# Kernel optimization log

Measured on AMD Instinct MI355X. Metric: run time of the kernel, lower is better.

The kernel has to match this reference:

```python
import jax, jax.numpy as jnp
import numpy as np

# Graph sizes: users -> items ('ui') and users -> tags ('ut'), plus reverse etypes.
N_U, N_I, N_T, D = 100000, 50000, 20000, 128
E_UI, E_UT = 500000, 300000


def setup_inputs() -> dict:
    key = jax.random.key(0)
    k = jax.random.split(key, 7)
    return {
        "h_u": jax.random.normal(k[0], (N_U, D), jnp.float32),
        "h_i": jax.random.normal(k[1], (N_I, D), jnp.float32),
        "h_t": jax.random.normal(k[2], (N_T, D), jnp.float32),
        "ui_src": jax.random.randint(k[3], (E_UI,), 0, N_U, jnp.int32),
        "ui_dst": jax.random.randint(k[4], (E_UI,), 0, N_I, jnp.int32),
        "ut_src": jax.random.randint(k[5], (E_UT,), 0, N_U, jnp.int32),
        "ut_dst": jax.random.randint(k[6], (E_UT,), 0, N_T, jnp.int32),
    }


def _seg_sum(x, idx, n):
    return jax.ops.segment_sum(x, idx, num_segments=n)


def _deg(idx, n):
    # in-degree, clamped to min 1 (as torch .clamp(min=1))
    return jnp.clip(_seg_sum(jnp.ones(idx.shape, jnp.float32), idx, n), 1.0, None)


def reference(h_u, h_i, h_t, ui_src, ui_dst, ut_src, ut_dst):
    NORM_2 = -1.0  # default norm_2 arg
    # forward pass: copy_u('h') + sum per etype, then 1/in_degree normalization on dst
    rst_i = _seg_sum(h_u[ui_src], ui_dst, N_I) / _deg(ui_dst, N_I)[:, None]  # [N_I, D]
    rst_t = _seg_sum(h_u[ut_src], ut_dst, N_T) / _deg(ut_dst, N_T)[:, None]  # [N_T, D]
    # backward pass: multi_update_all over reverse etypes, 'sum' cross-etype reducer
    bsrc = _seg_sum(rst_i[ui_dst], ui_src, N_U) + _seg_sum(rst_t[ut_dst], ut_src, N_U)
    # in_degrees_b: per-etype clamped degrees summed across reverse etypes
    deg_b = _deg(ui_src, N_U) + _deg(ut_src, N_U)
    bsrc = bsrc * (deg_b ** NORM_2)[:, None]
    # rst is the LAST etype's normalized dst result ('ut' -> tags)
    return bsrc, rst_t
```

## Files before the change

### kernel.cpp

```cpp
#include <hip/hip_runtime.h>

#define NU 100000
#define NI 50000
#define NT 20000
#define DD 128
#define EUI 500000
#define EUT 300000

#define B_I   0
#define B_T   (NI)
#define B_UUI (NI + NT)
#define B_UUT (NI + NT + NU)
#define NSCAN (NI + NT + NU + NU)
#define TOTAL_E (2 * (EUI + EUT))

#define BPB   512
#define NB    ((NSCAN + BPB - 1) / BPB)
#define CH    2048
#define NBLK  ((TOTAL_E + CH - 1) / CH)
#define NT3   176
#define NCVT  ((NU * DD / 8 + 255) / 256)

__device__ __forceinline__ unsigned bfpack(float a, float b) {
    unsigned ua = __float_as_uint(a), ub = __float_as_uint(b);
    ua = (ua + 0x7FFFu + ((ua >> 16) & 1u)) >> 16;
    ub = (ub + 0x7FFFu + ((ub >> 16) & 1u)) >> 16;
    return ua | (ub << 16);
}
__device__ __forceinline__ void bacc(unsigned p, float& a, float& b) {
    a += __uint_as_float(p << 16);
    b += __uint_as_float(p & 0xFFFF0000u);
}

typedef float f4_t __attribute__((ext_vector_type(4)));
__device__ __forceinline__ void nts4(float4* p, float x, float y, float z, float w) {
    f4_t v; v.x = x; v.y = y; v.z = z; v.w = w;
    __builtin_nontemporal_store(v, reinterpret_cast<f4_t*>(p));
}

__device__ __forceinline__ int bucket_of(int e,
        const int* __restrict__ ui_src, const int* __restrict__ ui_dst,
        const int* __restrict__ ut_src, const int* __restrict__ ut_dst) {
    if (e < EUI)               return B_I   + ui_dst[e];
    if (e < 2 * EUI)           return B_UUI + ui_src[e - EUI];
    if (e < 2 * EUI + EUT)     return B_T   + ut_dst[e - 2 * EUI];
    return B_UUT + ut_src[e - 2 * EUI - EUT];
}

__device__ __forceinline__ void entry_of(int e,
        const int* __restrict__ ui_src, const int* __restrict__ ui_dst,
        const int* __restrict__ ut_src, const int* __restrict__ ut_dst,
        int& bucket, int& val) {
    if (e < EUI)               { bucket = B_I   + ui_dst[e];               val = ui_src[e]; }
    else if (e < 2 * EUI)      { int j = e - EUI;           bucket = B_UUI + ui_src[j]; val = ui_dst[j]; }
    else if (e < 2 * EUI + EUT){ int j = e - 2 * EUI;       bucket = B_T   + ut_dst[j]; val = ut_src[j]; }
    else                       { int j = e - 2 * EUI - EUT; bucket = B_UUT + ut_src[j]; val = ut_dst[j]; }
}

__global__ void k_cvthist(const float4* __restrict__ in, uint4* __restrict__ out,
                          const int* __restrict__ ui_src, const int* __restrict__ ui_dst,
                          const int* __restrict__ ut_src, const int* __restrict__ ut_dst,
                          int* __restrict__ gbin) {
    __shared__ int h[NB];
    if (blockIdx.x < NCVT) {
        int t = blockIdx.x * 256 + threadIdx.x;
        if (t < NU * DD / 8) {
            float4 a = in[t * 2 + 0];
            float4 b = in[t * 2 + 1];
            uint4 o;
            o.x = bfpack(a.x, a.y); o.y = bfpack(a.z, a.w);
            o.z = bfpack(b.x, b.y); o.w = bfpack(b.z, b.w);
            out[t] = o;
        }
        return;
    }
    int b = blockIdx.x - NCVT, t = threadIdx.x;
    for (int i = t; i < NB; i += 256) h[i] = 0;
    __syncthreads();
    int e0 = b * CH;
    int e1 = min(e0 + CH, TOTAL_E);
    for (int e = e0 + t; e < e1; e += 256)
        atomicAdd(&h[bucket_of(e, ui_src, ui_dst, ut_src, ut_dst) >> 9], 1);
    __syncthreads();
    for (int i = t; i < NB; i += 256)
        if (h[i]) atomicAdd(&gbin[i], h[i]);
}

__global__ void k_scan528(const int* __restrict__ gbin,
                          int* __restrict__ gstart, int* __restrict__ cursor) {
    __shared__ int tsum[256];
    int t = threadIdx.x;
    int i = t * 3;
    int v0 = 0, v1 = 0, v2 = 0;
    if (t < NT3) { v0 = gbin[i]; v1 = gbin[i + 1]; v2 = gbin[i + 2]; }
    int s = v0 + v1 + v2;
    tsum[t] = s;
    __syncthreads();
    for (int o = 1; o < 256; o <<= 1) {
        int x = (t >= o) ? tsum[t - o] : 0;
        __syncthreads();
        tsum[t] += x;
        __syncthreads();
    }
    int base = tsum[t] - s;
    if (t < NT3) {
        gstart[i] = base;                cursor[i] = base;
        gstart[i + 1] = base + v0;       cursor[i + 1] = base + v0;
        gstart[i + 2] = base + v0 + v1;  cursor[i + 2] = base + v0 + v1;
    }
    if (t == 255) gstart[NB] = tsum[255];
}

__global__ void k_scatterbin2(const int* __restrict__ ui_src, const int* __restrict__ ui_dst,
                              const int* __restrict__ ut_src, const int* __restrict__ ut_dst,
                              int* __restrict__ cursor, unsigned* __restrict__ binned) {
    __shared__ int h[NB];
    int b = blockIdx.x, t = threadIdx.x;
    for (int i = t; i < NB; i += 256) h[i] = 0;
    __syncthreads();
    int e0 = b * CH;
    int e1 = min(e0 + CH, TOTAL_E);
    for (int e = e0 + t; e < e1; e += 256)
        atomicAdd(&h[bucket_of(e, ui_src, ui_dst, ut_src, ut_dst) >> 9], 1);
    __syncthreads();
    for (int i = t; i < NB; i += 256) {
        int c = h[i];
        if (c) h[i] = atomicAdd(&cursor[i], c);
    }
    __syncthreads();
    for (int e = e0 + t; e < e1; e += 256) {
        int bucket, val;
        entry_of(e, ui_src, ui_dst, ut_src, ut_dst, bucket, val);
        int pos = atomicAdd(&h[bucket >> 9], 1);
        binned[pos] = ((unsigned)(bucket & (BPB - 1)) << 17) | (unsigned)val;
    }
}

__global__ void k_fine(const unsigned* __restrict__ binned, const int* __restrict__ gstart,
                       int* __restrict__ off, int* __restrict__ edges) {
    __shared__ int cnt[BPB];
    __shared__ int tsum[256];
    int b = blockIdx.x, t = threadIdx.x;
    cnt[t] = 0; cnt[t + 256] = 0;
    __syncthreads();
    int s = gstart[b], e = gstart[b + 1];
    for (int i = s + t; i < e; i += 256) atomicAdd(&cnt[binned[i] >> 17], 1);
    __syncthreads();
    int v0 = cnt[2 * t], v1 = cnt[2 * t + 1];
    int ps = v0 + v1;
    tsum[t] = ps;
    __syncthreads();
    for (int o = 1; o < 256; o <<= 1) {
        int x = (t >= o) ? tsum[t - o] : 0;
        __syncthreads();
        tsum[t] += x;
        __syncthreads();
    }
    int base = s + tsum[t] - ps;
    int g0 = b * BPB + 2 * t;
    if (g0 < NSCAN) off[g0] = base;
    if (g0 + 1 < NSCAN) off[g0 + 1] = base + v0;
    __syncthreads();
    cnt[2 * t] = base;
    cnt[2 * t + 1] = base + v0;
    __syncthreads();
    for (int i = s + t; i < e; i += 256) {
        unsigned v = binned[i];
        int pos = atomicAdd(&cnt[v >> 17], 1);
        edges[pos] = (int)(v & 0x1FFFFu);
    }
}

__device__ __forceinline__ void gacc16(const uint4* __restrict__ feat,
                                       const int* __restrict__ edges,
                                       int start, int end, int c,
                                       float& a0, float& a1, float& a2, float& a3,
                                       float& a4, float& a5, float& a6, float& a7) {
    for (int base = start; base < end; base += 16) {
        int n = end - base; if (n > 16) n = 16;
        int eidx = (c < n) ? edges[base + c] : 0;
        int k = 0;
        for (; k + 8 <= n; k += 8) {
            int s0 = __shfl(eidx, k + 0, 16), s1 = __shfl(eidx, k + 1, 16);
            int s2 = __shfl(eidx, k + 2, 16), s3 = __shfl(eidx, k + 3, 16);
            int s4 = __shfl(eidx, k + 4, 16), s5 = __shfl(eidx, k + 5, 16);
            int s6 = __shfl(eidx, k + 6, 16), s7 = __shfl(eidx, k + 7, 16);
            uint4 p0 = feat[(size_t)s0 * 16 + c], p1 = feat[(size_t)s1 * 16 + c];
            uint4 p2 = feat[(size_t)s2 * 16 + c], p3 = feat[(size_t)s3 * 16 + c];
            uint4 p4 = feat[(size_t)s4 * 16 + c], p5 = feat[(size_t)s5 * 16 + c];
            uint4 p6 = feat[(size_t)s6 * 16 + c], p7 = feat[(size_t)s7 * 16 + c];
            bacc(p0.x, a0, a1); bacc(p0.y, a2, a3); bacc(p0.z, a4, a5); bacc(p0.w, a6, a7);
            bacc(p1.x, a0, a1); bacc(p1.y, a2, a3); bacc(p1.z, a4, a5); bacc(p1.w, a6, a7);
            bacc(p2.x, a0, a1); bacc(p2.y, a2, a3); bacc(p2.z, a4, a5); bacc(p2.w, a6, a7);
            bacc(p3.x, a0, a1); bacc(p3.y, a2, a3); bacc(p3.z, a4, a5); bacc(p3.w, a6, a7);
            bacc(p4.x, a0, a1); bacc(p4.y, a2, a3); bacc(p4.z, a4, a5); bacc(p4.w, a6, a7);
            bacc(p5.x, a0, a1); bacc(p5.y, a2, a3); bacc(p5.z, a4, a5); bacc(p5.w, a6, a7);
            bacc(p6.x, a0, a1); bacc(p6.y, a2, a3); bacc(p6.z, a4, a5); bacc(p6.w, a6, a7);
            bacc(p7.x, a0, a1); bacc(p7.y, a2, a3); bacc(p7.z, a4, a5); bacc(p7.w, a6, a7);
        }
        for (; k + 2 <= n; k += 2) {
            int s0 = __shfl(eidx, k + 0, 16), s1 = __shfl(eidx, k + 1, 16);
            uint4 p0 = feat[(size_t)s0 * 16 + c], p1 = feat[(size_t)s1 * 16 + c];
            bacc(p0.x, a0, a1); bacc(p0.y, a2, a3); bacc(p0.z, a4, a5); bacc(p0.w, a6, a7);
            bacc(p1.x, a0, a1); bacc(p1.y, a2, a3); bacc(p1.z, a4, a5); bacc(p1.w, a6, a7);
        }
        if (k < n) {
            int s0 = __shfl(eidx, k, 16);
            uint4 p0 = feat[(size_t)s0 * 16 + c];
            bacc(p0.x, a0, a1); bacc(p0.y, a2, a3); bacc(p0.z, a4, a5); bacc(p0.w, a6, a7);
        }
    }
}

__global__ void g_fwd(const uint4* __restrict__ feat,
                      const int* __restrict__ off, const int* __restrict__ edges,
                      uint4* __restrict__ rsti_b, uint4* __restrict__ rstt_b,
                      float4* __restrict__ outf) {
    int tid = blockIdx.x * blockDim.x + threadIdx.x;
    int r = tid >> 4;
    int c = tid & 15;
    if (r >= NI + NT) return;
    int start = off[r];
    int end = off[r + 1];
    float a0=0.f,a1=0.f,a2=0.f,a3=0.f,a4=0.f,a5=0.f,a6=0.f,a7=0.f;
    gacc16(feat, edges, start, end, c, a0, a1, a2, a3, a4, a5, a6, a7);
    float inv = 1.0f / fmaxf((float)(end - start), 1.0f);
    a0*=inv; a1*=inv; a2*=inv; a3*=inv; a4*=inv; a5*=inv; a6*=inv; a7*=inv;
    uint4 ob;
    ob.x = bfpack(a0,a1); ob.y = bfpack(a2,a3);
    ob.z = bfpack(a4,a5); ob.w = bfpack(a6,a7);
    if (r < NI) {
        rsti_b[(size_t)r * 16 + c] = ob;
    } else {
        int rt = r - NI;
        rstt_b[(size_t)rt * 16 + c] = ob;
        nts4(&outf[(size_t)rt * 32 + c*2 + 0], a0, a1, a2, a3);
        nts4(&outf[(size_t)rt * 32 + c*2 + 1], a4, a5, a6, a7);
    }
}

__global__ void g_bwd(const uint4* __restrict__ rst_i, const uint4* __restrict__ rst_t,
                      const int* __restrict__ off, const int* __restrict__ edges,
                      float4* __restrict__ bsrc) {
    int tid = blockIdx.x * blockDim.x + threadIdx.x;
    int r = tid >> 4;
    int c = tid & 15;
    if (r >= NU) return;
    int s1 = off[B_UUI + r], e1 = off[B_UUI + r + 1];
    int g2 = B_UUT + r;
    int s2 = off[g2], e2 = (g2 + 1 < NSCAN) ? off[g2 + 1] : TOTAL_E;
    float a0=0.f,a1=0.f,a2=0.f,a3=0.f,a4=0.f,a5=0.f,a6=0.f,a7=0.f;
    gacc16(rst_i, edges, s1, e1, c, a0, a1, a2, a3, a4, a5, a6, a7);
    gacc16(rst_t, edges, s2, e2, c, a0, a1, a2, a3, a4, a5, a6, a7);
    float inv = 1.0f / (fmaxf((float)(e1 - s1), 1.0f) + fmaxf((float)(e2 - s2), 1.0f));
    nts4(&bsrc[(size_t)r * 32 + c*2 + 0], a0*inv, a1*inv, a2*inv, a3*inv);
    nts4(&bsrc[(size_t)r * 32 + c*2 + 1], a4*inv, a5*inv, a6*inv, a7*inv);
}

__global__ void k_scanA(int* __restrict__ data, int* __restrict__ bsums, int n) {
    __shared__ int lds[256];
    int b = blockIdx.x, t = threadIdx.x;
    int base = b * 1024 + t * 4;
    int v0 = (base + 0 < n) ? data[base + 0] : 0;
    int v1 = (base + 1 < n) ? data[base + 1] : 0;
    int v2 = (base + 2 < n) ? data[base + 2] : 0;
    int v3 = (base + 3 < n) ? data[base + 3] : 0;
    int i0 = v0, i1 = i0 + v1, i2 = i1 + v2, i3 = i2 + v3;
    lds[t] = i3;
    __syncthreads();
    for (int o = 1; o < 256; o <<= 1) {
        int x = (t >= o) ? lds[t - o] : 0;
        __syncthreads();
        lds[t] += x;
        __syncthreads();
    }
    int ex = lds[t] - i3;
    if (base + 0 < n) data[base + 0] = ex + i0;
    if (base + 1 < n) data[base + 1] = ex + i1;
    if (base + 2 < n) data[base + 2] = ex + i2;
    if (base + 3 < n) data[base + 3] = ex + i3;
    if (t == 255) bsums[b] = lds[255];
}

__global__ void k_scanB(int* __restrict__ bsums, int nsb) {
    __shared__ int lds[512];
    int t = threadIdx.x;
    int a = (t < nsb) ? bsums[t] : 0;
    int b2 = (t + 256 < nsb) ? bsums[t + 256] : 0;
    lds[t] = a;
    lds[t + 256] = b2;
    __syncthreads();
    for (int o = 1; o < 512; o <<= 1) {
        int x0 = (t >= o) ? lds[t - o] : 0;
        int x1 = (t + 256 >= o) ? lds[t + 256 - o] : 0;
        __syncthreads();
        lds[t] += x0;
        lds[t + 256] += x1;
        __syncthreads();
    }
    if (t < nsb) bsums[t] = lds[t] - a;
    if (t + 256 < nsb) bsums[t + 256] = lds[t + 256] - b2;
}

__global__ void k_scanC(int* __restrict__ data, const int* __restrict__ bsums, int n) {
    int b = blockIdx.x;
    int add = bsums[b];
    int base = b * 1024 + threadIdx.x * 4;
    if (base + 0 < n) data[base + 0] += add;
    if (base + 1 < n) data[base + 1] += add;
    if (base + 2 < n) data[base + 2] += add;
    if (base + 3 < n) data[base + 3] += add;
}

__global__ void k_count_old(const int4* __restrict__ ui_src, const int4* __restrict__ ui_dst,
                            const int4* __restrict__ ut_src, const int4* __restrict__ ut_dst,
                            int* __restrict__ off) {
    int i = blockIdx.x * blockDim.x + threadIdx.x;
    if (i < EUI / 4) {
        int4 s = ui_src[i], d = ui_dst[i];
        atomicAdd(&off[B_I + d.x], 1); atomicAdd(&off[B_I + d.y], 1);
        atomicAdd(&off[B_I + d.z], 1); atomicAdd(&off[B_I + d.w], 1);
        atomicAdd(&off[B_UUI + s.x], 1); atomicAdd(&off[B_UUI + s.y], 1);
        atomicAdd(&off[B_UUI + s.z], 1); atomicAdd(&off[B_UUI + s.w], 1);
    } else if (i < EUI / 4 + EUT / 4) {
        int j = i - EUI / 4;
        int4 s = ut_src[j], d = ut_dst[j];
        atomicAdd(&off[B_T + d.x], 1); atomicAdd(&off[B_T + d.y], 1);
        atomicAdd(&off[B_T + d.z], 1); atomicAdd(&off[B_T + d.w], 1);
        atomicAdd(&off[B_UUT + s.x], 1); atomicAdd(&off[B_UUT + s.y], 1);
        atomicAdd(&off[B_UUT + s.z], 1); atomicAdd(&off[B_UUT + s.w], 1);
    }
}

__global__ void k_fill_old(const int2* __restrict__ ui_src, const int2* __restrict__ ui_dst,
                           const int2* __restrict__ ut_src, const int2* __restrict__ ut_dst,
                           int* __restrict__ off, int* __restrict__ edges) {
    int i = blockIdx.x * blockDim.x + threadIdx.x;
    if (i < EUI / 2) {
        int2 s = ui_src[i], d = ui_dst[i];
        edges[atomicAdd(&off[B_I + d.x], -1) - 1] = s.x;
        edges[atomicAdd(&off[B_UUI + s.x], -1) - 1] = d.x;
        edges[atomicAdd(&off[B_I + d.y], -1) - 1] = s.y;
        edges[atomicAdd(&off[B_UUI + s.y], -1) - 1] = d.y;
    } else if (i < EUI / 2 + EUT / 2) {
        int j = i - EUI / 2;
        int2 s = ut_src[j], d = ut_dst[j];
        edges[atomicAdd(&off[B_T + d.x], -1) - 1] = s.x;
        edges[atomicAdd(&off[B_UUT + s.x], -1) - 1] = d.x;
        edges[atomicAdd(&off[B_T + d.y], -1) - 1] = s.y;
        edges[atomicAdd(&off[B_UUT + s.y], -1) - 1] = d.y;
    }
}

__global__ void k_gather_fwd_f(const float4* __restrict__ feat,
                               const int* __restrict__ off, const int* __restrict__ edges,
                               uint2* __restrict__ outb, float4* __restrict__ outf,
                               int base, int nrows) {
    int tid = blockIdx.x * blockDim.x + threadIdx.x;
    int r = tid >> 5;
    int c = tid & 31;
    if (r >= nrows) return;
    int g = base + r;
    int start = off[g];
    int end = (g + 1 < NSCAN) ? off[g + 1] : TOTAL_E;
    float a0 = 0.f, a1 = 0.f, a2 = 0.f, a3 = 0.f;
    for (int e = start; e < end; ++e) {
        float4 v = feat[(size_t)edges[e] * 32 + c];
        a0 += v.x; a1 += v.y; a2 += v.z; a3 += v.w;
    }
    float inv = 1.0f / fmaxf((float)(end - start), 1.0f);
    a0 *= inv; a1 *= inv; a2 *= inv; a3 *= inv;
    uint2 ob; ob.x = bfpack(a0, a1); ob.y = bfpack(a2, a3);
    outb[(size_t)r * 32 + c] = ob;
    if (outf) {
        float4 of; of.x = a0; of.y = a1; of.z = a2; of.w = a3;
        outf[(size_t)r * 32 + c] = of;
    }
}

__global__ void k_gather_bwd_b(const uint2* __restrict__ rst_i,
                               const uint2* __restrict__ rst_t,
                               const int* __restrict__ off, const int* __restrict__ edges,
                               float4* __restrict__ bsrc) {
    int tid = blockIdx.x * blockDim.x + threadIdx.x;
    int r = tid >> 5;
    int c = tid & 31;
    if (r >= NU) return;
    int g1 = B_UUI + r;
    int s1 = off[g1], e1 = off[g1 + 1];
    int g2 = B_UUT + r;
    int s2 = off[g2], e2 = (g2 + 1 < NSCAN) ? off[g2 + 1] : TOTAL_E;
    float a0 = 0.f, a1 = 0.f, a2 = 0.f, a3 = 0.f;
    for (int e = s1; e < e1; ++e) {
        uint2 p = rst_i[(size_t)edges[e] * 32 + c];
        bacc(p.x, a0, a1); bacc(p.y, a2, a3);
    }
    for (int e = s2; e < e2; ++e) {
        uint2 p = rst_t[(size_t)edges[e] * 32 + c];
        bacc(p.x, a0, a1); bacc(p.y, a2, a3);
    }
    float inv = 1.0f / (fmaxf((float)(e1 - s1), 1.0f) + fmaxf((float)(e2 - s2), 1.0f));
    float4 o;
    o.x = a0 * inv; o.y = a1 * inv; o.z = a2 * inv; o.w = a3 * inv;
    bsrc[(size_t)r * 32 + c] = o;
}

__global__ void f_count(const int* __restrict__ ui_src, const int* __restrict__ ui_dst,
                        const int* __restrict__ ut_src, const int* __restrict__ ut_dst,
                        float* __restrict__ cnt_uui, float* __restrict__ cnt_i,
                        float* __restrict__ cnt_uut, float* __restrict__ cnt_t) {
    int i = blockIdx.x * blockDim.x + threadIdx.x;
    if (i < EUI) {
        unsafeAtomicAdd(&cnt_uui[ui_src[i]], 1.0f);
        unsafeAtomicAdd(&cnt_i[ui_dst[i]], 1.0f);
    } else if (i < EUI + EUT) {
        int j = i - EUI;
        unsafeAtomicAdd(&cnt_uut[ut_src[j]], 1.0f);
        unsafeAtomicAdd(&cnt_t[ut_dst[j]], 1.0f);
    }
}
__global__ void f_scatter_fwd(const float4* __restrict__ feat, const int* __restrict__ src,
                              const int* __restrict__ dst, float* __restrict__ out_sum, int nedge) {
    int tid = blockIdx.x * blockDim.x + threadIdx.x;
    int e = tid >> 5, c = tid & 31;
    if (e >= nedge) return;
    float4 v = feat[(size_t)src[e] * 32 + c];
    float* o = out_sum + (size_t)dst[e] * DD + c * 4;
    unsafeAtomicAdd(o + 0, v.x); unsafeAtomicAdd(o + 1, v.y);
    unsafeAtomicAdd(o + 2, v.z); unsafeAtomicAdd(o + 3, v.w);
}
__global__ void f_scatter_bwd(const float4* __restrict__ rst_sum, const float* __restrict__ cnt,
                              const int* __restrict__ src, const int* __restrict__ dst,
                              float* __restrict__ bsrc, int nedge) {
    int tid = blockIdx.x * blockDim.x + threadIdx.x;
    int e = tid >> 5, c = tid & 31;
    if (e >= nedge) return;
    float inv = 1.0f / fmaxf(cnt[dst[e]], 1.0f);
    float4 v = rst_sum[(size_t)dst[e] * 32 + c];
    float* o = bsrc + (size_t)src[e] * DD + c * 4;
    unsafeAtomicAdd(o + 0, v.x * inv); unsafeAtomicAdd(o + 1, v.y * inv);
    unsafeAtomicAdd(o + 2, v.z * inv); unsafeAtomicAdd(o + 3, v.w * inv);
}
__global__ void f_norm(float4* __restrict__ rst, const float* __restrict__ cnt, int nrows) {
    int tid = blockIdx.x * blockDim.x + threadIdx.x;
    int r = tid >> 5, c = tid & 31;
    if (r >= nrows) return;
    float inv = 1.0f / fmaxf(cnt[r], 1.0f);
    float4 v = rst[(size_t)r * 32 + c];
    v.x *= inv; v.y *= inv; v.z *= inv; v.w *= inv;
    rst[(size_t)r * 32 + c] = v;
}
__global__ void f_final(float4* __restrict__ bsrc, const float* __restrict__ cnt_a,
                        const float* __restrict__ cnt_b, int nrows) {
    int tid = blockIdx.x * blockDim.x + threadIdx.x;
    int r = tid >> 5, c = tid & 31;
    if (r >= nrows) return;
    float inv = 1.0f / (fmaxf(cnt_a[r], 1.0f) + fmaxf(cnt_b[r], 1.0f));
    float4 v = bsrc[(size_t)r * 32 + c];
    v.x *= inv; v.y *= inv; v.z *= inv; v.w *= inv;
    bsrc[(size_t)r * 32 + c] = v;
}


extern "C" void kernel_launch(void* const* d_in, const int* in_sizes, int n_in,
                              void* d_out, int out_size, void* d_ws, size_t ws_size,
                              hipStream_t stream) {
    const float* h_u  = (const float*)d_in[0];
    const int* ui_src = (const int*)d_in[3];
    const int* ui_dst = (const int*)d_in[4];
    const int* ut_src = (const int*)d_in[5];
    const int* ut_dst = (const int*)d_in[6];

    float* bsrc  = (float*)d_out;
    float* rst_t = (float*)d_out + (size_t)NU * DD;

    const int B = 256;

    const size_t INT_WORDS = (size_t)NSCAN + 512 + TOTAL_E;
    const size_t BASE_B    = INT_WORDS * 4;
    const size_t HUB_B     = (size_t)NU * DD * 2;
    const size_t RIB_B     = (size_t)NI * DD * 2;
    const size_t RTB_B     = (size_t)NT * DD * 2;
    const size_t NEED_FULL = BASE_B + HUB_B + RIB_B + RTB_B;
    const size_t NEED_HALF = BASE_B + RIB_B + RTB_B;

    if (ws_size >= NEED_FULL) {
        int* off      = (int*)d_ws;
        int* bsums    = off + NSCAN;   (void)bsums;
        int* edges    = bsums + 512;
        uint4* hu_b   = (uint4*)((char*)d_ws + BASE_B);
        uint4* rsti_b = (uint4*)((char*)d_ws + BASE_B + HUB_B);
        uint4* rstt_b = (uint4*)((char*)d_ws + BASE_B + HUB_B + RIB_B);
        unsigned* binned = (unsigned*)rsti_b;
        int* gbin   = (int*)rstt_b;
        int* gstart = gbin + NB;
        int* cursor = gstart + NB + 1;

        hipMemsetAsync(gbin, 0, NB * sizeof(int), stream);

        k_cvthist<<<NCVT + NBLK, B, 0, stream>>>(
            (const float4*)h_u, hu_b, ui_src, ui_dst, ut_src, ut_dst, gbin);

        k_scan528<<<1, B, 0, stream>>>(gbin, gstart, cursor);

        k_scatterbin2<<<NBLK, B, 0, stream>>>(ui_src, ui_dst, ut_src, ut_dst, cursor, binned);

        k_fine<<<NB, B, 0, stream>>>(binned, gstart, off, edges);

        g_fwd<<<((long)(NI + NT) * 16 + B - 1) / B, B, 0, stream>>>(
            hu_b, off, edges, rsti_b, rstt_b, (float4*)rst_t);
        g_bwd<<<((long)NU * 16 + B - 1) / B, B, 0, stream>>>(
            rsti_b, rstt_b, off, edges, (float4*)bsrc);
    } else if (ws_size >= NEED_HALF) {
        int* off   = (int*)d_ws;
        int* bsums = off + NSCAN;
        int* edges = bsums + 512;
        uint2* rsti_b = (uint2*)((char*)d_ws + BASE_B);
        uint2* rstt_b = (uint2*)((char*)d_ws + BASE_B + RIB_B);

        hipMemsetAsync(off, 0, (NSCAN + 512) * sizeof(int), stream);

        int nq = EUI / 4 + EUT / 4;
        k_count_old<<<(nq + B - 1) / B, B, 0, stream>>>(
            (const int4*)ui_src, (const int4*)ui_dst,
            (const int4*)ut_src, (const int4*)ut_dst, off);
        {
            int nblk = (NSCAN + 1023) / 1024;
            k_scanA<<<nblk, B, 0, stream>>>(off, bsums, NSCAN);
            k_scanB<<<1, B, 0, stream>>>(bsums, nblk);
            k_scanC<<<nblk, B, 0, stream>>>(off, bsums, NSCAN);
        }
        int nh = EUI / 2 + EUT / 2;
        k_fill_old<<<(nh + B - 1) / B, B, 0, stream>>>(
            (const int2*)ui_src, (const int2*)ui_dst,
            (const int2*)ut_src, (const int2*)ut_dst, off, edges);

        k_gather_fwd_f<<<((long)NI * 32 + B - 1) / B, B, 0, stream>>>(
            (const float4*)h_u, off, edges, rsti_b, (float4*)nullptr, B_I, NI);
        k_gather_fwd_f<<<((long)NT * 32 + B - 1) / B, B, 0, stream>>>(
            (const float4*)h_u, off, edges, rstt_b, (float4*)rst_t, B_T, NT);
        k_gather_bwd_b<<<((long)NU * 32 + B - 1) / B, B, 0, stream>>>(
            rsti_b, rstt_b, off, edges, (float4*)bsrc);
    } else {
        float* ws        = (float*)d_ws;
        float* rst_i_sum = ws;
        float* cnt_i     = rst_i_sum + (size_t)NI * DD;
        float* cnt_t     = cnt_i + NI;
        float* cnt_uui   = cnt_t + NT;
        float* cnt_uut   = cnt_uui + NU;
        size_t ws_floats = (size_t)NI * DD + NI + NT + NU + NU;

        hipMemsetAsync(d_ws, 0, ws_floats * sizeof(float), stream);
        hipMemsetAsync(d_out, 0, (size_t)out_size * sizeof(float), stream);

        int n = EUI + EUT;
        f_count<<<(n + B - 1) / B, B, 0, stream>>>(ui_src, ui_dst, ut_src, ut_dst,
                                                   cnt_uui, cnt_i, cnt_uut, cnt_t);
        f_scatter_fwd<<<((long)EUI * 32 + B - 1) / B, B, 0, stream>>>(
            (const float4*)h_u, ui_src, ui_dst, rst_i_sum, EUI);
        f_scatter_fwd<<<((long)EUT * 32 + B - 1) / B, B, 0, stream>>>(
            (const float4*)h_u, ut_src, ut_dst, rst_t, EUT);
        f_scatter_bwd<<<((long)EUI * 32 + B - 1) / B, B, 0, stream>>>(
            (const float4*)rst_i_sum, cnt_i, ui_src, ui_dst, bsrc, EUI);
        f_scatter_bwd<<<((long)EUT * 32 + B - 1) / B, B, 0, stream>>>(
            (const float4*)rst_t, cnt_t, ut_src, ut_dst, bsrc, EUT);
        f_norm<<<((long)NT * 32 + B - 1) / B, B, 0, stream>>>((float4*)rst_t, cnt_t, NT);
        f_final<<<((long)NU * 32 + B - 1) / B, B, 0, stream>>>((float4*)bsrc, cnt_uui, cnt_uut, NU);
    }
}
```

Before: 159.6 us.

## Merge per-user ui and ut backward buckets into one CSR segment

Each user now gets a single CSR bucket holding both reverse etypes' edges, with tag neighbours offset by NI so one gather loop reads from the contiguous rst_i/rst_t bf16 buffers. Per-etype degrees are recovered by ballot/popcount of indices below NI. This shrinks the scan from 528 to 333 bins, halves the user offset array and removes the second gather loop with its tail handling, so short user segments pack better. The code relies on rsti_b and rstt_b being adjacent in the workspace, and NSCAN still sizes the workspace layout.

Result: slower. 165.9 us (+4.0%).

```diff
diff --git a/kernel.cpp b/kernel.cpp
--- a/kernel.cpp
+++ b/kernel.cpp
@@ -9,16 +9,19 @@
 
 #define B_I   0
 #define B_T   (NI)
+#define B_U   (NI + NT)
+#define NSCAN2 (NI + NT + NU)
+#define TOTAL_E (2 * (EUI + EUT))
+
 #define B_UUI (NI + NT)
 #define B_UUT (NI + NT + NU)
 #define NSCAN (NI + NT + NU + NU)
-#define TOTAL_E (2 * (EUI + EUT))
 
 #define BPB   512
-#define NB    ((NSCAN + BPB - 1) / BPB)
+#define NB2   ((NSCAN2 + BPB - 1) / BPB)
 #define CH    2048
 #define NBLK  ((TOTAL_E + CH - 1) / CH)
-#define NT3   176
+#define NT3   111
 #define NCVT  ((NU * DD / 8 + 255) / 256)
 
 __device__ __forceinline__ unsigned bfpack(float a, float b) {
@@ -41,27 +44,27 @@
 __device__ __forceinline__ int bucket_of(int e,
         const int* __restrict__ ui_src, const int* __restrict__ ui_dst,
         const int* __restrict__ ut_src, const int* __restrict__ ut_dst) {
-    if (e < EUI)               return B_I   + ui_dst[e];
-    if (e < 2 * EUI)           return B_UUI + ui_src[e - EUI];
-    if (e < 2 * EUI + EUT)     return B_T   + ut_dst[e - 2 * EUI];
-    return B_UUT + ut_src[e - 2 * EUI - EUT];
+    if (e < EUI)               return B_I + ui_dst[e];
+    if (e < 2 * EUI)           return B_U + ui_src[e - EUI];
+    if (e < 2 * EUI + EUT)     return B_T + ut_dst[e - 2 * EUI];
+    return B_U + ut_src[e - 2 * EUI - EUT];
 }
 
 __device__ __forceinline__ void entry_of(int e,
         const int* __restrict__ ui_src, const int* __restrict__ ui_dst,
         const int* __restrict__ ut_src, const int* __restrict__ ut_dst,
         int& bucket, int& val) {
-    if (e < EUI)               { bucket = B_I   + ui_dst[e];               val = ui_src[e]; }
-    else if (e < 2 * EUI)      { int j = e - EUI;           bucket = B_UUI + ui_src[j]; val = ui_dst[j]; }
-    else if (e < 2 * EUI + EUT){ int j = e - 2 * EUI;       bucket = B_T   + ut_dst[j]; val = ut_src[j]; }
-    else                       { int j = e - 2 * EUI - EUT; bucket = B_UUT + ut_src[j]; val = ut_dst[j]; }
+    if (e < EUI)               { bucket = B_I + ui_dst[e];                 val = ui_src[e]; }
+    else if (e < 2 * EUI)      { int j = e - EUI;           bucket = B_U + ui_src[j]; val = ui_dst[j]; }
+    else if (e < 2 * EUI + EUT){ int j = e - 2 * EUI;       bucket = B_T + ut_dst[j]; val = ut_src[j]; }
+    else                       { int j = e - 2 * EUI - EUT; bucket = B_U + ut_src[j]; val = NI + ut_dst[j]; }
 }
 
 __global__ void k_cvthist(const float4* __restrict__ in, uint4* __restrict__ out,
                           const int* __restrict__ ui_src, const int* __restrict__ ui_dst,
                           const int* __restrict__ ut_src, const int* __restrict__ ut_dst,
                           int* __restrict__ gbin) {
-    __shared__ int h[NB];
+    __shared__ int h[NB2];
     if (blockIdx.x < NCVT) {
         int t = blockIdx.x * 256 + threadIdx.x;
         if (t < NU * DD / 8) {
@@ -75,18 +78,18 @@
         return;
     }
     int b = blockIdx.x - NCVT, t = threadIdx.x;
-    for (int i = t; i < NB; i += 256) h[i] = 0;
+    for (int i = t; i < NB2; i += 256) h[i] = 0;
     __syncthreads();
     int e0 = b * CH;
     int e1 = min(e0 + CH, TOTAL_E);
     for (int e = e0 + t; e < e1; e += 256)
         atomicAdd(&h[bucket_of(e, ui_src, ui_dst, ut_src, ut_dst) >> 9], 1);
     __syncthreads();
-    for (int i = t; i < NB; i += 256)
+    for (int i = t; i < NB2; i += 256)
         if (h[i]) atomicAdd(&gbin[i], h[i]);
 }
 
-__global__ void k_scan528(const int* __restrict__ gbin,
+__global__ void k_scan333(const int* __restrict__ gbin,
                           int* __restrict__ gstart, int* __restrict__ cursor) {
     __shared__ int tsum[256];
     int t = threadIdx.x;
@@ -108,22 +111,22 @@
         gstart[i + 1] = base + v0;       cursor[i + 1] = base + v0;
         gstart[i + 2] = base + v0 + v1;  cursor[i + 2] = base + v0 + v1;
     }
-    if (t == 255) gstart[NB] = tsum[255];
+    if (t == 255) gstart[NB2] = tsum[255];
 }
 
 __global__ void k_scatterbin2(const int* __restrict__ ui_src, const int* __restrict__ ui_dst,
                               const int* __restrict__ ut_src, const int* __restrict__ ut_dst,
                               int* __restrict__ cursor, unsigned* __restrict__ binned) {
-    __shared__ int h[NB];
+    __shared__ int h[NB2];
     int b = blockIdx.x, t = threadIdx.x;
-    for (int i = t; i < NB; i += 256) h[i] = 0;
+    for (int i = t; i < NB2; i += 256) h[i] = 0;
     __syncthreads();
     int e0 = b * CH;
     int e1 = min(e0 + CH, TOTAL_E);
     for (int e = e0 + t; e < e1; e += 256)
         atomicAdd(&h[bucket_of(e, ui_src, ui_dst, ut_src, ut_dst) >> 9], 1);
     __syncthreads();
-    for (int i = t; i < NB; i += 256) {
+    for (int i = t; i < NB2; i += 256) {
         int c = h[i];
         if (c) h[i] = atomicAdd(&cursor[i], c);
     }
@@ -158,8 +161,8 @@
     }
     int base = s + tsum[t] - ps;
     int g0 = b * BPB + 2 * t;
-    if (g0 < NSCAN) off[g0] = base;
-    if (g0 + 1 < NSCAN) off[g0 + 1] = base + v0;
+    if (g0 < NSCAN2) off[g0] = base;
+    if (g0 + 1 < NSCAN2) off[g0 + 1] = base + v0;
     __syncthreads();
     cnt[2 * t] = base;
     cnt[2 * t + 1] = base + v0;
@@ -239,20 +242,58 @@
     }
 }
 
-__global__ void g_bwd(const uint4* __restrict__ rst_i, const uint4* __restrict__ rst_t,
+__global__ void g_bwd(const uint4* __restrict__ rst,
                       const int* __restrict__ off, const int* __restrict__ edges,
                       float4* __restrict__ bsrc) {
     int tid = blockIdx.x * blockDim.x + threadIdx.x;
     int r = tid >> 4;
     int c = tid & 15;
     if (r >= NU) return;
-    int s1 = off[B_UUI + r], e1 = off[B_UUI + r + 1];
-    int g2 = B_UUT + r;
-    int s2 = off[g2], e2 = (g2 + 1 < NSCAN) ? off[g2 + 1] : TOTAL_E;
+    int g = B_U + r;
+    int s = off[g];
+    int e = (g + 1 < NSCAN2) ? off[g + 1] : TOTAL_E;
+    int gsh = threadIdx.x & 48;
+    int nui = 0;
     float a0=0.f,a1=0.f,a2=0.f,a3=0.f,a4=0.f,a5=0.f,a6=0.f,a7=0.f;
-    gacc16(rst_i, edges, s1, e1, c, a0, a1, a2, a3, a4, a5, a6, a7);
-    gacc16(rst_t, edges, s2, e2, c, a0, a1, a2, a3, a4, a5, a6, a7);
-    float inv = 1.0f / (fmaxf((float)(e1 - s1), 1.0f) + fmaxf((float)(e2 - s2), 1.0f));
+    for (int base = s; base < e; base += 16) {
+        int n = e - base; if (n > 16) n = 16;
+        int eidx = (c < n) ? edges[base + c] : 0x7FFFFFFF;
+        unsigned long long m = __ballot((c < n) && (eidx < NI));
+        nui += (int)__popcll((m >> gsh) & 0xFFFFull);
+        int k = 0;
+        for (; k + 8 <= n; k += 8) {
+            int s0 = __shfl(eidx, k + 0, 16), s1 = __shfl(eidx, k + 1, 16);
+            int s2 = __shfl(eidx, k + 2, 16), s3 = __shfl(eidx, k + 3, 16);
+            int s4 = __shfl(eidx, k + 4, 16), s5 = __shfl(eidx, k + 5, 16);
+            int s6 = __shfl(eidx, k + 6, 16), s7 = __shfl(eidx, k + 7, 16);
+            uint4 p0 = rst[(size_t)s0 * 16 + c], p1 = rst[(size_t)s1 * 16 + c];
+            uint4 p2 = rst[(size_t)s2 * 16 + c], p3 = rst[(size_t)s3 * 16 + c];
+            uint4 p4 = rst[(size_t)s4 * 16 + c], p5 = rst[(size_t)s5 * 16 + c];
+            uint4 p6 = rst[(size_t)s6 * 16 + c], p7 = rst[(size_t)s7 * 16 + c];
+            bacc(p0.x, a0, a1); bacc(p0.y, a2, a3); bacc(p0.z, a4, a5); bacc(p0.w, a6, a7);
+            bacc(p1.x, a0, a1); bacc(p1.y, a2, a3); bacc(p1.z, a4, a5); bacc(p1.w, a6, a7);
+            bacc(p2.x, a0, a1); bacc(p2.y, a2, a3); bacc(p2.z, a4, a5); bacc(p2.w, a6, a7);
+            bacc(p3.x, a0, a1); bacc(p3.y, a2, a3); bacc(p3.z, a4, a5); bacc(p3.w, a6, a7);
+            bacc(p4.x, a0, a1); bacc(p4.y, a2, a3); bacc(p4.z, a4, a5); bacc(p4.w, a6, a7);
+            bacc(p5.x, a0, a1); bacc(p5.y, a2, a3); bacc(p5.z, a4, a5); bacc(p5.w, a6, a7);
+            bacc(p6.x, a0, a1); bacc(p6.y, a2, a3); bacc(p6.z, a4, a5); bacc(p6.w, a6, a7);
+            bacc(p7.x, a0, a1); bacc(p7.y, a2, a3); bacc(p7.z, a4, a5); bacc(p7.w, a6, a7);
+        }
+        for (; k + 2 <= n; k += 2) {
+            int s0 = __shfl(eidx, k + 0, 16), s1 = __shfl(eidx, k + 1, 16);
+            uint4 p0 = rst[(size_t)s0 * 16 + c], p1 = rst[(size_t)s1 * 16 + c];
+            bacc(p0.x, a0, a1); bacc(p0.y, a2, a3); bacc(p0.z, a4, a5); bacc(p0.w, a6, a7);
+            bacc(p1.x, a0, a1); bacc(p1.y, a2, a3); bacc(p1.z, a4, a5); bacc(p1.w, a6, a7);
+        }
+        if (k < n) {
+            int s0 = __shfl(eidx, k, 16);
+            uint4 p0 = rst[(size_t)s0 * 16 + c];
+            bacc(p0.x, a0, a1); bacc(p0.y, a2, a3); bacc(p0.z, a4, a5); bacc(p0.w, a6, a7);
+        }
+    }
+    int ntot = e - s;
+    float denom = fmaxf((float)nui, 1.0f) + fmaxf((float)(ntot - nui), 1.0f);
+    float inv = 1.0f / denom;
     nts4(&bsrc[(size_t)r * 32 + c*2 + 0], a0*inv, a1*inv, a2*inv, a3*inv);
     nts4(&bsrc[(size_t)r * 32 + c*2 + 1], a4*inv, a5*inv, a6*inv, a7*inv);
 }
@@ -493,24 +534,24 @@
         uint4* rstt_b = (uint4*)((char*)d_ws + BASE_B + HUB_B + RIB_B);
         unsigned* binned = (unsigned*)rsti_b;
         int* gbin   = (int*)rstt_b;
-        int* gstart = gbin + NB;
-        int* cursor = gstart + NB + 1;
-
-        hipMemsetAsync(gbin, 0, NB * sizeof(int), stream);
+        int* gstart = gbin + NB2;
+        int* cursor = gstart + NB2 + 1;
+
+        hipMemsetAsync(gbin, 0, NB2 * sizeof(int), stream);
 
         k_cvthist<<<NCVT + NBLK, B, 0, stream>>>(
             (const float4*)h_u, hu_b, ui_src, ui_dst, ut_src, ut_dst, gbin);
 
-        k_scan528<<<1, B, 0, stream>>>(gbin, gstart, cursor);
+        k_scan333<<<1, B, 0, stream>>>(gbin, gstart, cursor);
 
         k_scatterbin2<<<NBLK, B, 0, stream>>>(ui_src, ui_dst, ut_src, ut_dst, cursor, binned);
 
-        k_fine<<<NB, B, 0, stream>>>(binned, gstart, off, edges);
+        k_fine<<<NB2, B, 0, stream>>>(binned, gstart, off, edges);
 
         g_fwd<<<((long)(NI + NT) * 16 + B - 1) / B, B, 0, stream>>>(
             hu_b, off, edges, rsti_b, rstt_b, (float4*)rst_t);
         g_bwd<<<((long)NU * 16 + B - 1) / B, B, 0, stream>>>(
-            rsti_b, rstt_b, off, edges, (float4*)bsrc);
+            rsti_b , off, edges, (float4*)bsrc);
     } else if (ws_size >= NEED_HALF) {
         int* off   = (int*)d_ws;
         int* bsums = off + NSCAN;
```
